# Performance work log

Measured on AMD Instinct MI355X. Metric: run time of the kernel, lower is better.

Reference implementation:

```python
import jax, jax.numpy as jnp
import numpy as np

CUBE_SIZE = 24
N_NEURONS = CUBE_SIZE ** 3  # 13824
INPUT_DIM = 512
OUTPUT_DIM = 1000
MAX_STEPS = 30
BATCH = 256


def _build_neighbor_indices(size: int) -> np.ndarray:
    """[N, 27] int32; invalid (out-of-cube) neighbors map to pad slot N."""
    n = size ** 3
    c = np.arange(size)
    z, y, x = np.meshgrid(c, c, c, indexing='ij')  # each [size,size,size]
    cols = []
    for dz in (-1, 0, 1):
        for dy in (-1, 0, 1):
            for dx in (-1, 0, 1):
                nz, ny, nx = z + dz, y + dy, x + dx
                valid = ((nz >= 0) & (nz < size) & (ny >= 0) & (ny < size)
                         & (nx >= 0) & (nx < size))
                idx = nz * size * size + ny * size + nx
                cols.append(np.where(valid, idx, n))
    return np.stack(cols, axis=-1).reshape(n, 27).astype(np.int32)


def setup_inputs() -> dict:
    key = jax.random.key(0)
    ks = jax.random.split(key, 4)
    # xavier-ish small init scales (gain 0.5 style)
    w_in = jax.random.normal(ks[0], (N_NEURONS, INPUT_DIM), jnp.float32) * 0.01
    w_local = jax.random.normal(ks[1], (N_NEURONS, 27), jnp.float32) * 0.1
    w_out = jax.random.normal(ks[2], (OUTPUT_DIM, N_NEURONS), jnp.float32) * 0.01
    x = jax.random.normal(ks[3], (BATCH, INPUT_DIM), jnp.float32)
    return {
        'x': x,
        'W_in_w': w_in,
        'W_in_b': jnp.zeros((N_NEURONS,), jnp.float32),
        'W_local': w_local,
        'W_out_w': w_out,
        'W_out_b': jnp.zeros((OUTPUT_DIM,), jnp.float32),
        'neighbor_indices': jnp.asarray(_build_neighbor_indices(CUBE_SIZE)),
    }


def reference(x, W_in_w, W_in_b, W_local, W_out_w, W_out_b, neighbor_indices):
    batch = x.shape[0]
    x_proj = x @ W_in_w.T + W_in_b  # [B, N]
    h0 = jnp.zeros((batch, N_NEURONS), x.dtype)
    pad = jnp.zeros((batch, 1), x.dtype)

    def step(h, _):
        h_padded = jnp.concatenate([h, pad], axis=1)        # [B, N+1]
        nbr = h_padded[:, neighbor_indices]                  # [B, N, 27]
        weighted = jnp.einsum('bnk,nk->bn', nbr, W_local)    # [B, N]
        return jnp.tanh(x_proj + weighted), None

    h, _ = jax.lax.scan(step, h0, None, length=MAX_STEPS)
    return h @ W_out_w.T + W_out_b  # [B, output_dim]
```

## Files before the change

kernel.cpp:

```cpp
#include <hip/hip_runtime.h>
#include <hip/hip_bf16.h>

#define NN   13824
#define BB   256
#define KDIM 512
#define ODIM 1000
#define CUBE 24
#define KS   16
#define ASTR 872

typedef short bf8 __attribute__((ext_vector_type(8)));
typedef float f32x4 __attribute__((ext_vector_type(4)));

__device__ __forceinline__ float fast_tanh(float a) {
    float e = __expf(2.0f * a);
    return 1.0f - 2.0f / (e + 1.0f);
}
__device__ __forceinline__ float bf_lo(unsigned u) { return __uint_as_float(u << 16); }
__device__ __forceinline__ float bf_hi(unsigned u) { return __uint_as_float(u & 0xffff0000u); }
__device__ __forceinline__ unsigned short bf_rne(float f) {
    unsigned u = __float_as_uint(f);
    u += 0x7fffu + ((u >> 16) & 1u);
    return (unsigned short)(u >> 16);
}
__device__ __forceinline__ unsigned pk_bf16(float lo, float hi) {
    union { __hip_bfloat162 h; unsigned u; } cv;
    cv.h = __float22bfloat162_rn(make_float2(lo, hi));
    return cv.u;
}
__device__ __forceinline__ bf8 cvt8(float4 a, float4 b) {
    union { bf8 v; unsigned u[4]; } r;
    r.u[0] = pk_bf16(a.x, a.y);
    r.u[1] = pk_bf16(a.z, a.w);
    r.u[2] = pk_bf16(b.x, b.y);
    r.u[3] = pk_bf16(b.z, b.w);
    return r.v;
}

__global__ __launch_bounds__(256) void xbf_kernel(
    const float* __restrict__ x, unsigned* __restrict__ xb)
{
    int i = blockIdx.x * 256 + threadIdx.x;
    float2 v = *(const float2*)&x[(size_t)i * 2];
    xb[i] = pk_bf16(v.x, v.y);
}

__global__ __launch_bounds__(256) void xproj_mfma(
    const float* __restrict__ w_in, const float* __restrict__ bias,
    const short* __restrict__ xbf, unsigned short* __restrict__ xp,
    unsigned short* __restrict__ h1)
{
    const int tid = threadIdx.x, w = tid >> 6, lane = tid & 63;
    const int quad = lane >> 4, l16 = lane & 15;
    const int n0 = blockIdx.x * 16;
    const float* __restrict__ arow = &w_in[(size_t)(n0 + l16) * KDIM];

    f32x4 acc[4] = {};

    int ka = quad * 8;
    float4 a0 = *(const float4*)&arow[ka];
    float4 a1 = *(const float4*)&arow[ka + 4];
    bf8 bb[4];
#pragma unroll
    for (int j = 0; j < 4; ++j)
        bb[j] = *(const bf8*)&xbf[(size_t)(w * 64 + j * 16 + l16) * KDIM + ka];

    for (int it = 0; it < 16; ++it) {
        float4 na0{}, na1{}; bf8 nb[4] = {};
        if (it < 15) {
            const int nka = ka + 32;
            na0 = *(const float4*)&arow[nka];
            na1 = *(const float4*)&arow[nka + 4];
#pragma unroll
            for (int j = 0; j < 4; ++j)
                nb[j] = *(const bf8*)&xbf[(size_t)(w * 64 + j * 16 + l16) * KDIM + nka];
        }
        bf8 af = cvt8(a0, a1);
#pragma unroll
        for (int j = 0; j < 4; ++j)
            acc[j] = __builtin_amdgcn_mfma_f32_16x16x32_bf16(af, bb[j], acc[j], 0, 0, 0);
        a0 = na0; a1 = na1;
#pragma unroll
        for (int j = 0; j < 4; ++j) bb[j] = nb[j];
        ka += 32;
    }

#pragma unroll
    for (int j = 0; j < 4; ++j) {
        const int b = w * 64 + j * 16 + l16;
#pragma unroll
        for (int r = 0; r < 4; ++r) {
            const int n = n0 + quad * 4 + r;
            const float v = acc[j][r] + bias[n];
            xp[(size_t)n * BB + b] = bf_rne(v);
            h1[(size_t)n * BB + b] = bf_rne(fast_tanh(v));
        }
    }
}

__device__ __forceinline__ void load_plane_f2(
    const unsigned* __restrict__ h32, int z, int y, int xx, int dof, float2* w9)
{
#pragma unroll
    for (int j = 0; j < 9; ++j) {
        const int dz = j / 3 - 1, dy = j % 3 - 1;
        const int zz = z + dz, yy = y + dy;
        const bool valid = (xx >= 0) & (xx < CUBE) & (zz >= 0) & (zz < CUBE) &
                           (yy >= 0) & (yy < CUBE);
        unsigned v = 0u;
        if (valid) v = h32[(size_t)((zz * 24 + yy) * 24 + xx) * 128 + dof];
        w9[j] = make_float2(bf_lo(v), bf_hi(v));
    }
}

__global__ __launch_bounds__(256) void step_kernel(
    const unsigned* __restrict__ hprev, const unsigned* __restrict__ xp,
    const float* __restrict__ wl, unsigned* __restrict__ hnext)
{
    const int tid  = threadIdx.x;
    const int wid  = __builtin_amdgcn_readfirstlane(tid >> 6);
    const int wvb  = wid & 1;
    const int yoff = wid >> 1;
    const int lane = tid & 63;

    const int bid   = blockIdx.x;
    const int zhi   = bid & 7;
    const int inner = bid >> 3;
    const int yp    = inner % 12;
    const int r     = inner / 12;
    const int xc    = r & 3;
    const int zlo   = r >> 2;
    const int z     = zhi * 3 + zlo;
    const int y     = yp * 2 + yoff;

    const int x0   = xc * 6;
    const int dof  = wvb * 64 + lane;

    float2 win[5][9];
    load_plane_f2(hprev, z, y, x0 - 1, dof, win[0]);
    load_plane_f2(hprev, z, y, x0,     dof, win[1]);
    load_plane_f2(hprev, z, y, x0 + 1, dof, win[2]);
    load_plane_f2(hprev, z, y, x0 + 2, dof, win[3]);

#pragma unroll
    for (int xi = 0; xi < 6; ++xi) {
        const int x = x0 + xi;
        if (xi <= 3)
            load_plane_f2(hprev, z, y, x + 3, dof, win[(xi + 4) % 5]);

        const int n = (z * 24 + y) * 24 + x;
        const float* __restrict__ wn = &wl[(size_t)n * 27];
        const unsigned xpv = xp[(size_t)n * 128 + dof];
        float2 acc = make_float2(bf_lo(xpv), bf_hi(xpv));

        const float2* pm = win[xi % 5];
        const float2* pc = win[(xi + 1) % 5];
        const float2* pp = win[(xi + 2) % 5];
#pragma unroll
        for (int j = 0; j < 9; ++j) {
            const float w0 = wn[3 * j + 0];
            const float w1 = wn[3 * j + 1];
            const float w2 = wn[3 * j + 2];
            acc.x += w0 * pm[j].x + w1 * pc[j].x + w2 * pp[j].x;
            acc.y += w0 * pm[j].y + w1 * pc[j].y + w2 * pp[j].y;
        }
        hnext[(size_t)n * 128 + dof] = pk_bf16(fast_tanh(acc.x), fast_tanh(acc.y));
    }
}

__global__ __launch_bounds__(256) void transpose_kernel(
    const unsigned* __restrict__ h32, unsigned* __restrict__ hT32)
{
    __shared__ unsigned short T[64][66];
    const int tid = threadIdx.x;
    const int rr = tid >> 2, g = tid & 3;
    const int k0 = blockIdx.x * 64, b0 = blockIdx.y * 64;
#pragma unroll
    for (int i = 0; i < 8; ++i) {
        unsigned d = h32[(size_t)(k0 + rr) * 128 + b0 / 2 + g * 8 + i];
        const int bl = (g * 8 + i) * 2;
        T[bl][rr]     = (unsigned short)(d & 0xffffu);
        T[bl + 1][rr] = (unsigned short)(d >> 16);
    }
    __syncthreads();
#pragma unroll
    for (int i = 0; i < 8; ++i) {
        const int kl = (g * 8 + i) * 2;
        unsigned d = (unsigned)T[rr][kl] | ((unsigned)T[rr][kl + 1] << 16);
        hT32[(size_t)(b0 + rr) * (NN / 2) + k0 / 2 + g * 8 + i] = d;
    }
}

__global__ __launch_bounds__(256) void outgemm_mfma(
    const float* __restrict__ wout, const short* __restrict__ hT,
    float* __restrict__ part)
{
    __shared__ unsigned short As[32 * ASTR];
    const int tid = threadIdx.x, w = tid >> 6, lane = tid & 63;
    const int quad = lane >> 4, l16 = lane & 15;
    const int kb = blockIdx.x * (NN / KS);
    const int o0 = blockIdx.y * 32;
    const int b0 = w * 64;

#pragma unroll
    for (int rr = 0; rr < 8; ++rr) {
        const int row = w * 8 + rr;
        const int o = o0 + row;
        const float* __restrict__ src = &wout[(size_t)o * NN + kb];
#pragma unroll
        for (int c = 0; c < 4; ++c) {
            const int col = c * 256 + lane * 4;
            if (c < 3 || lane < 24) {
                float4 v = {0.f, 0.f, 0.f, 0.f};
                if (o < ODIM) v = *(const float4*)&src[col];
                uint2 pk2 = make_uint2(pk_bf16(v.x, v.y), pk_bf16(v.z, v.w));
                *(uint2*)&As[(unsigned)row * ASTR + (unsigned)col] = pk2;
            }
        }
    }
    __syncthreads();

    f32x4 acc[2][4] = {};

    bf8 bb[4];
    {
        const int ka = kb + quad * 8;
#pragma unroll
        for (int j = 0; j < 4; ++j)
            bb[j] = *(const bf8*)&hT[(size_t)(b0 + j * 16 + l16) * NN + ka];
    }

    const int r0 = l16, r1 = 16 + l16;

    for (int kc = 0; kc < 27; ++kc) {
        bf8 nb[4] = {};
        if (kc < 26) {
            const int ka = kb + (kc + 1) * 32 + quad * 8;
#pragma unroll
            for (int j = 0; j < 4; ++j)
                nb[j] = *(const bf8*)&hT[(size_t)(b0 + j * 16 + l16) * NN + ka];
        }
        const int cs = kc * 32 + quad * 8;
        bf8 a0 = *(const bf8*)&As[(unsigned)r0 * ASTR + (unsigned)cs];
        bf8 a1 = *(const bf8*)&As[(unsigned)r1 * ASTR + (unsigned)cs];
#pragma unroll
        for (int j = 0; j < 4; ++j) {
            acc[0][j] = __builtin_amdgcn_mfma_f32_16x16x32_bf16(a0, bb[j], acc[0][j], 0, 0, 0);
            acc[1][j] = __builtin_amdgcn_mfma_f32_16x16x32_bf16(a1, bb[j], acc[1][j], 0, 0, 0);
        }
#pragma unroll
        for (int j = 0; j < 4; ++j) bb[j] = nb[j];
    }

#pragma unroll
    for (int i = 0; i < 2; ++i)
#pragma unroll
        for (int j = 0; j < 4; ++j) {
            const int b = b0 + j * 16 + l16;
#pragma unroll
            for (int r = 0; r < 4; ++r) {
                const int o = o0 + i * 16 + quad * 4 + r;
                part[((size_t)blockIdx.x * 1024 + o) * BB + b] = acc[i][j][r];
            }
        }
}

__global__ __launch_bounds__(256) void reduce_kernel(
    const float* __restrict__ part, const float* __restrict__ bias,
    float* __restrict__ out)
{
    const int o = blockIdx.x, b = threadIdx.x;
    float s = bias[o];
#pragma unroll
    for (int kc = 0; kc < KS; ++kc)
        s += part[((size_t)kc * 1024 + o) * BB + b];
    out[(size_t)b * ODIM + o] = s;
}

extern "C" void kernel_launch(void* const* d_in, const int* in_sizes, int n_in,
                              void* d_out, int out_size, void* d_ws, size_t ws_size,
                              hipStream_t stream)
{
    const float* x       = (const float*)d_in[0];
    const float* w_in    = (const float*)d_in[1];
    const float* b_in    = (const float*)d_in[2];
    const float* w_local = (const float*)d_in[3];
    const float* w_out   = (const float*)d_in[4];
    const float* b_out   = (const float*)d_in[5];
    float* out = (float*)d_out;

    char* p = (char*)d_ws;
    unsigned short* xp_bf = (unsigned short*)p;          p += (size_t)NN * BB * 2;
    unsigned short* hA    = (unsigned short*)p;          p += (size_t)NN * BB * 2;
    unsigned short* hB    = (unsigned short*)p;          p += (size_t)NN * BB * 2;
    unsigned short* hT    = (unsigned short*)p;          p += (size_t)NN * BB * 2;
    unsigned short* x_bf  = (unsigned short*)p;          p += (size_t)BB * KDIM * 2;
    float*          part  = (float*)p;

    xbf_kernel<<<256, 256, 0, stream>>>(x, (unsigned*)x_bf);
    xproj_mfma<<<864, 256, 0, stream>>>(w_in, b_in, (const short*)x_bf, xp_bf, hA);

    const unsigned* hp = (const unsigned*)hA;
    unsigned* hn = (unsigned*)hB;
    for (int s = 0; s < 29; ++s) {
        step_kernel<<<1152, 256, 0, stream>>>(hp, (const unsigned*)xp_bf, w_local, hn);
        unsigned* t = (unsigned*)hp; hp = hn; hn = t;
    }

    transpose_kernel<<<dim3(216, 4), 256, 0, stream>>>(hp, (unsigned*)hT);
    outgemm_mfma<<<dim3(KS, 32), 256, 0, stream>>>(w_out, (const short*)hT, part);
    reduce_kernel<<<ODIM, 256, 0, stream>>>(part, b_out, out);
}
```

Baseline: 552.9 us.

## Stage 3D halo tiles of hidden state in LDS for stencil step

The step kernel now loads a 6x6x6 halo tile (4x4x4 interior) of the previous hidden state for 64 batch pairs into shared memory, then each wave computes one z-slice of the tile from LDS. This replaces the old per-thread global sliding-window loads, cutting redundant global reads of neighbours. The grid drops from 1152 to 432 blocks, which may reduce occupancy and parallelism, and the 54 KB LDS tile limits blocks per CU. Separately, the xproj kernel converts its W_in row block to bf16 once into LDS instead of converting in registers inside the loop.

Result: slower. 986.3 us (+78.4%).

```diff
diff --git a/kernel.cpp b/kernel.cpp
--- a/kernel.cpp
+++ b/kernel.cpp
@@ -8,6 +8,7 @@
 #define CUBE 24
 #define KS   16
 #define ASTR 872
+#define XSTR 520
 
 typedef short bf8 __attribute__((ext_vector_type(8)));
 typedef float f32x4 __attribute__((ext_vector_type(4)));
@@ -28,14 +29,6 @@
     cv.h = __float22bfloat162_rn(make_float2(lo, hi));
     return cv.u;
 }
-__device__ __forceinline__ bf8 cvt8(float4 a, float4 b) {
-    union { bf8 v; unsigned u[4]; } r;
-    r.u[0] = pk_bf16(a.x, a.y);
-    r.u[1] = pk_bf16(a.z, a.w);
-    r.u[2] = pk_bf16(b.x, b.y);
-    r.u[3] = pk_bf16(b.z, b.w);
-    return r.v;
-}
 
 __global__ __launch_bounds__(256) void xbf_kernel(
     const float* __restrict__ x, unsigned* __restrict__ xb)
@@ -50,36 +43,45 @@
     const short* __restrict__ xbf, unsigned short* __restrict__ xp,
     unsigned short* __restrict__ h1)
 {
+    __shared__ unsigned short As[16 * XSTR];
     const int tid = threadIdx.x, w = tid >> 6, lane = tid & 63;
     const int quad = lane >> 4, l16 = lane & 15;
     const int n0 = blockIdx.x * 16;
-    const float* __restrict__ arow = &w_in[(size_t)(n0 + l16) * KDIM];
+
+#pragma unroll
+    for (int rr = 0; rr < 4; ++rr) {
+        const int row = w * 4 + rr;
+        const float* __restrict__ src = &w_in[(size_t)(n0 + row) * KDIM];
+#pragma unroll
+        for (int c = 0; c < 2; ++c) {
+            const int col = c * 256 + lane * 4;
+            float4 v = *(const float4*)&src[col];
+            uint2 pk2 = make_uint2(pk_bf16(v.x, v.y), pk_bf16(v.z, v.w));
+            *(uint2*)&As[row * XSTR + col] = pk2;
+        }
+    }
+    __syncthreads();
 
     f32x4 acc[4] = {};
 
     int ka = quad * 8;
-    float4 a0 = *(const float4*)&arow[ka];
-    float4 a1 = *(const float4*)&arow[ka + 4];
     bf8 bb[4];
 #pragma unroll
     for (int j = 0; j < 4; ++j)
         bb[j] = *(const bf8*)&xbf[(size_t)(w * 64 + j * 16 + l16) * KDIM + ka];
 
     for (int it = 0; it < 16; ++it) {
-        float4 na0{}, na1{}; bf8 nb[4] = {};
+        bf8 nb[4] = {};
         if (it < 15) {
             const int nka = ka + 32;
-            na0 = *(const float4*)&arow[nka];
-            na1 = *(const float4*)&arow[nka + 4];
 #pragma unroll
             for (int j = 0; j < 4; ++j)
                 nb[j] = *(const bf8*)&xbf[(size_t)(w * 64 + j * 16 + l16) * KDIM + nka];
         }
-        bf8 af = cvt8(a0, a1);
+        bf8 af = *(const bf8*)&As[l16 * XSTR + it * 32 + quad * 8];
 #pragma unroll
         for (int j = 0; j < 4; ++j)
             acc[j] = __builtin_amdgcn_mfma_f32_16x16x32_bf16(af, bb[j], acc[j], 0, 0, 0);
-        a0 = na0; a1 = na1;
 #pragma unroll
         for (int j = 0; j < 4; ++j) bb[j] = nb[j];
         ka += 32;
@@ -98,17 +100,14 @@
     }
 }
 
-__device__ __forceinline__ void load_plane_f2(
-    const unsigned* __restrict__ h32, int z, int y, int xx, int dof, float2* w9)
+__device__ __forceinline__ void ldplane_lds(
+    const unsigned* __restrict__ Ls, int zo, int yo, int p, int lane,
+    float2* w9)
 {
 #pragma unroll
     for (int j = 0; j < 9; ++j) {
-        const int dz = j / 3 - 1, dy = j % 3 - 1;
-        const int zz = z + dz, yy = y + dy;
-        const bool valid = (xx >= 0) & (xx < CUBE) & (zz >= 0) & (zz < CUBE) &
-                           (yy >= 0) & (yy < CUBE);
-        unsigned v = 0u;
-        if (valid) v = h32[(size_t)((zz * 24 + yy) * 24 + xx) * 128 + dof];
+        const int dz = j / 3, dy = j % 3;
+        const unsigned v = Ls[(((zo + dz) * 6 + (yo + dy)) * 6 + p) * 64 + lane];
         w9[j] = make_float2(bf_lo(v), bf_hi(v));
     }
 }
@@ -117,54 +116,66 @@
     const unsigned* __restrict__ hprev, const unsigned* __restrict__ xp,
     const float* __restrict__ wl, unsigned* __restrict__ hnext)
 {
+    __shared__ unsigned Ls[216 * 64];
     const int tid  = threadIdx.x;
-    const int wid  = __builtin_amdgcn_readfirstlane(tid >> 6);
-    const int wvb  = wid & 1;
-    const int yoff = wid >> 1;
+    const int w    = __builtin_amdgcn_readfirstlane(tid >> 6);
     const int lane = tid & 63;
 
-    const int bid   = blockIdx.x;
-    const int zhi   = bid & 7;
-    const int inner = bid >> 3;
-    const int yp    = inner % 12;
-    const int r     = inner / 12;
-    const int xc    = r & 3;
-    const int zlo   = r >> 2;
-    const int z     = zhi * 3 + zlo;
-    const int y     = yp * 2 + yoff;
-
-    const int x0   = xc * 6;
-    const int dof  = wvb * 64 + lane;
-
+    const int bid  = blockIdx.x;
+    const int half = bid & 1;
+    const int t    = bid >> 1;
+    const int tx   = t % 6;
+    const int ty   = (t / 6) % 6;
+    const int tz   = t / 36;
+    const int z0 = tz * 4, y0 = ty * 4, x0 = tx * 4;
+    const int dof = half * 64 + lane;
+
+#pragma unroll 6
+    for (int i = 0; i < 54; ++i) {
+        const int r  = w * 54 + i;
+        const int lx = r % 6, ly = (r / 6) % 6, lz = r / 36;
+        const int z = z0 - 1 + lz, y = y0 - 1 + ly, x = x0 - 1 + lx;
+        const bool valid = (z >= 0) & (z < CUBE) & (y >= 0) & (y < CUBE) &
+                           (x >= 0) & (x < CUBE);
+        unsigned v = 0u;
+        if (valid) v = hprev[(size_t)((z * 24 + y) * 24 + x) * 128 + dof];
+        Ls[r * 64 + lane] = v;
+    }
+    __syncthreads();
+
+    const int zo = w;
     float2 win[5][9];
-    load_plane_f2(hprev, z, y, x0 - 1, dof, win[0]);
-    load_plane_f2(hprev, z, y, x0,     dof, win[1]);
-    load_plane_f2(hprev, z, y, x0 + 1, dof, win[2]);
-    load_plane_f2(hprev, z, y, x0 + 2, dof, win[3]);
-
-#pragma unroll
-    for (int xi = 0; xi < 6; ++xi) {
-        const int x = x0 + xi;
-        if (xi <= 3)
-            load_plane_f2(hprev, z, y, x + 3, dof, win[(xi + 4) % 5]);
-
-        const int n = (z * 24 + y) * 24 + x;
-        const float* __restrict__ wn = &wl[(size_t)n * 27];
-        const unsigned xpv = xp[(size_t)n * 128 + dof];
-        float2 acc = make_float2(bf_lo(xpv), bf_hi(xpv));
-
-        const float2* pm = win[xi % 5];
-        const float2* pc = win[(xi + 1) % 5];
-        const float2* pp = win[(xi + 2) % 5];
-#pragma unroll
-        for (int j = 0; j < 9; ++j) {
-            const float w0 = wn[3 * j + 0];
-            const float w1 = wn[3 * j + 1];
-            const float w2 = wn[3 * j + 2];
-            acc.x += w0 * pm[j].x + w1 * pc[j].x + w2 * pp[j].x;
-            acc.y += w0 * pm[j].y + w1 * pc[j].y + w2 * pp[j].y;
-        }
-        hnext[(size_t)n * 128 + dof] = pk_bf16(fast_tanh(acc.x), fast_tanh(acc.y));
+#pragma unroll 1
+    for (int yo = 0; yo < 4; ++yo) {
+        ldplane_lds(Ls, zo, yo, 0, lane, win[0]);
+        ldplane_lds(Ls, zo, yo, 1, lane, win[1]);
+        ldplane_lds(Ls, zo, yo, 2, lane, win[2]);
+        ldplane_lds(Ls, zo, yo, 3, lane, win[3]);
+
+#pragma unroll
+        for (int xo = 0; xo < 4; ++xo) {
+            if (xo <= 1)
+                ldplane_lds(Ls, zo, yo, xo + 4, lane, win[(xo + 4) % 5]);
+
+            const int n = ((z0 + zo) * 24 + (y0 + yo)) * 24 + (x0 + xo);
+            const float* __restrict__ wn = &wl[(size_t)n * 27];
+            const unsigned xpv = xp[(size_t)n * 128 + dof];
+            float2 acc = make_float2(bf_lo(xpv), bf_hi(xpv));
+
+            const float2* pm = win[xo % 5];
+            const float2* pc = win[(xo + 1) % 5];
+            const float2* pp = win[(xo + 2) % 5];
+#pragma unroll
+            for (int j = 0; j < 9; ++j) {
+                const float w0 = wn[3 * j + 0];
+                const float w1 = wn[3 * j + 1];
+                const float w2 = wn[3 * j + 2];
+                acc.x += w0 * pm[j].x + w1 * pc[j].x + w2 * pp[j].x;
+                acc.y += w0 * pm[j].y + w1 * pc[j].y + w2 * pp[j].y;
+            }
+            hnext[(size_t)n * 128 + dof] =
+                pk_bf16(fast_tanh(acc.x), fast_tanh(acc.y));
+        }
     }
 }
 
@@ -303,7 +314,7 @@
     const unsigned* hp = (const unsigned*)hA;
     unsigned* hn = (unsigned*)hB;
     for (int s = 0; s < 29; ++s) {
-        step_kernel<<<1152, 256, 0, stream>>>(hp, (const unsigned*)xp_bf, w_local, hn);
+        step_kernel<<<432, 256, 0, stream>>>(hp, (const unsigned*)xp_bf, w_local, hn);
         unsigned* t = (unsigned*)hp; hp = hn; hn = t;
     }
 
```

## Stage W_in through LDS in xproj and retile output GEMM to 128-row blocks

Applied to the files above, without the earlier changes.

In xproj, each block now loads its 16 W_in rows coalesced, converts them to bf16 once into shared memory, and feeds the MFMAs from LDS instead of strided per-lane global loads. The output GEMM is restructured to 512-thread blocks covering 128 output rows, with the weight tile staged in two K phases so it fits in LDS. Each hT fragment now feeds 8 MFMA row tiles, cutting redundant hT reads. The cost is fewer blocks (128 instead of 512), an extra barrier between phases, and more accumulator registers per thread.

After: 553.8 us. Within noise of the previous version (+0.1%).

```diff
diff --git a/kernel.cpp b/kernel.cpp
--- a/kernel.cpp
+++ b/kernel.cpp
@@ -7,7 +7,8 @@
 #define ODIM 1000
 #define CUBE 24
 #define KS   16
-#define ASTR 872
+#define XSTR 520
+#define OSTR 456
 
 typedef short bf8 __attribute__((ext_vector_type(8)));
 typedef float f32x4 __attribute__((ext_vector_type(4)));
@@ -28,14 +29,6 @@
     cv.h = __float22bfloat162_rn(make_float2(lo, hi));
     return cv.u;
 }
-__device__ __forceinline__ bf8 cvt8(float4 a, float4 b) {
-    union { bf8 v; unsigned u[4]; } r;
-    r.u[0] = pk_bf16(a.x, a.y);
-    r.u[1] = pk_bf16(a.z, a.w);
-    r.u[2] = pk_bf16(b.x, b.y);
-    r.u[3] = pk_bf16(b.z, b.w);
-    return r.v;
-}
 
 __global__ __launch_bounds__(256) void xbf_kernel(
     const float* __restrict__ x, unsigned* __restrict__ xb)
@@ -50,36 +43,45 @@
     const short* __restrict__ xbf, unsigned short* __restrict__ xp,
     unsigned short* __restrict__ h1)
 {
+    __shared__ unsigned short As[16 * XSTR];
     const int tid = threadIdx.x, w = tid >> 6, lane = tid & 63;
     const int quad = lane >> 4, l16 = lane & 15;
     const int n0 = blockIdx.x * 16;
-    const float* __restrict__ arow = &w_in[(size_t)(n0 + l16) * KDIM];
+
+#pragma unroll
+    for (int rr = 0; rr < 4; ++rr) {
+        const int row = w * 4 + rr;
+        const float* __restrict__ src = &w_in[(size_t)(n0 + row) * KDIM];
+#pragma unroll
+        for (int c = 0; c < 2; ++c) {
+            const int col = c * 256 + lane * 4;
+            float4 v = *(const float4*)&src[col];
+            uint2 pk2 = make_uint2(pk_bf16(v.x, v.y), pk_bf16(v.z, v.w));
+            *(uint2*)&As[row * XSTR + col] = pk2;
+        }
+    }
+    __syncthreads();
 
     f32x4 acc[4] = {};
 
     int ka = quad * 8;
-    float4 a0 = *(const float4*)&arow[ka];
-    float4 a1 = *(const float4*)&arow[ka + 4];
     bf8 bb[4];
 #pragma unroll
     for (int j = 0; j < 4; ++j)
         bb[j] = *(const bf8*)&xbf[(size_t)(w * 64 + j * 16 + l16) * KDIM + ka];
 
     for (int it = 0; it < 16; ++it) {
-        float4 na0{}, na1{}; bf8 nb[4] = {};
+        bf8 nb[4] = {};
         if (it < 15) {
             const int nka = ka + 32;
-            na0 = *(const float4*)&arow[nka];
-            na1 = *(const float4*)&arow[nka + 4];
 #pragma unroll
             for (int j = 0; j < 4; ++j)
                 nb[j] = *(const bf8*)&xbf[(size_t)(w * 64 + j * 16 + l16) * KDIM + nka];
         }
-        bf8 af = cvt8(a0, a1);
+        bf8 af = *(const bf8*)&As[l16 * XSTR + it * 32 + quad * 8];
 #pragma unroll
         for (int j = 0; j < 4; ++j)
             acc[j] = __builtin_amdgcn_mfma_f32_16x16x32_bf16(af, bb[j], acc[j], 0, 0, 0);
-        a0 = na0; a1 = na1;
 #pragma unroll
         for (int j = 0; j < 4; ++j) bb[j] = nb[j];
         ka += 32;
@@ -191,76 +193,83 @@
     }
 }
 
-__global__ __launch_bounds__(256) void outgemm_mfma(
+__global__ __launch_bounds__(512) void outgemm_mfma(
     const float* __restrict__ wout, const short* __restrict__ hT,
     float* __restrict__ part)
 {
-    __shared__ unsigned short As[32 * ASTR];
+    __shared__ unsigned short As[128 * OSTR];
     const int tid = threadIdx.x, w = tid >> 6, lane = tid & 63;
     const int quad = lane >> 4, l16 = lane & 15;
     const int kb = blockIdx.x * (NN / KS);
-    const int o0 = blockIdx.y * 32;
-    const int b0 = w * 64;
-
-#pragma unroll
-    for (int rr = 0; rr < 8; ++rr) {
-        const int row = w * 8 + rr;
-        const int o = o0 + row;
-        const float* __restrict__ src = &wout[(size_t)o * NN + kb];
-#pragma unroll
-        for (int c = 0; c < 4; ++c) {
-            const int col = c * 256 + lane * 4;
-            if (c < 3 || lane < 24) {
+    const int o0 = blockIdx.y * 128;
+    const int b0 = w * 32;
+
+    f32x4 acc[8][2] = {};
+
+#pragma unroll 1
+    for (int ph = 0; ph < 2; ++ph) {
+        const int poff  = ph ? 448 : 0;
+        const int pcols = ph ? 416 : 448;
+        const int pkc   = ph ? 13 : 14;
+        if (ph) __syncthreads();
+
+#pragma unroll 4
+        for (int rr = 0; rr < 16; ++rr) {
+            const int row = w * 16 + rr;
+            const int o = o0 + row;
+            const float* __restrict__ src = &wout[(size_t)o * NN + kb + poff];
+            {
+                const int col = lane * 4;
                 float4 v = {0.f, 0.f, 0.f, 0.f};
                 if (o < ODIM) v = *(const float4*)&src[col];
-                uint2 pk2 = make_uint2(pk_bf16(v.x, v.y), pk_bf16(v.z, v.w));
-                *(uint2*)&As[(unsigned)row * ASTR + (unsigned)col] = pk2;
-            }
-        }
-    }
-    __syncthreads();
-
-    f32x4 acc[2][4] = {};
-
-    bf8 bb[4];
-    {
-        const int ka = kb + quad * 8;
-#pragma unroll
-        for (int j = 0; j < 4; ++j)
-            bb[j] = *(const bf8*)&hT[(size_t)(b0 + j * 16 + l16) * NN + ka];
-    }
-
-    const int r0 = l16, r1 = 16 + l16;
-
-    for (int kc = 0; kc < 27; ++kc) {
-        bf8 nb[4] = {};
-        if (kc < 26) {
-            const int ka = kb + (kc + 1) * 32 + quad * 8;
-#pragma unroll
-            for (int j = 0; j < 4; ++j)
-                nb[j] = *(const bf8*)&hT[(size_t)(b0 + j * 16 + l16) * NN + ka];
-        }
-        const int cs = kc * 32 + quad * 8;
-        bf8 a0 = *(const bf8*)&As[(unsigned)r0 * ASTR + (unsigned)cs];
-        bf8 a1 = *(const bf8*)&As[(unsigned)r1 * ASTR + (unsigned)cs];
-#pragma unroll
-        for (int j = 0; j < 4; ++j) {
-            acc[0][j] = __builtin_amdgcn_mfma_f32_16x16x32_bf16(a0, bb[j], acc[0][j], 0, 0, 0);
-            acc[1][j] = __builtin_amdgcn_mfma_f32_16x16x32_bf16(a1, bb[j], acc[1][j], 0, 0, 0);
-        }
-#pragma unroll
-        for (int j = 0; j < 4; ++j) bb[j] = nb[j];
-    }
-
-#pragma unroll
-    for (int i = 0; i < 2; ++i)
-#pragma unroll
-        for (int j = 0; j < 4; ++j) {
+                *(uint2*)&As[row * OSTR + col] =
+                    make_uint2(pk_bf16(v.x, v.y), pk_bf16(v.z, v.w));
+            }
+            {
+                const int col = 256 + lane * 4;
+                if (col < pcols) {
+                    float4 v = {0.f, 0.f, 0.f, 0.f};
+                    if (o < ODIM) v = *(const float4*)&src[col];
+                    *(uint2*)&As[row * OSTR + col] =
+                        make_uint2(pk_bf16(v.x, v.y), pk_bf16(v.z, v.w));
+                }
+            }
+        }
+        __syncthreads();
+
+        bf8 b0f, b1f;
+        {
+            const int ka = kb + poff + quad * 8;
+            b0f = *(const bf8*)&hT[(size_t)(b0 + l16) * NN + ka];
+            b1f = *(const bf8*)&hT[(size_t)(b0 + 16 + l16) * NN + ka];
+        }
+        for (int kc = 0; kc < pkc; ++kc) {
+            bf8 n0 = {}, n1 = {};
+            if (kc + 1 < pkc) {
+                const int ka = kb + poff + (kc + 1) * 32 + quad * 8;
+                n0 = *(const bf8*)&hT[(size_t)(b0 + l16) * NN + ka];
+                n1 = *(const bf8*)&hT[(size_t)(b0 + 16 + l16) * NN + ka];
+            }
+            const int cs = kc * 32 + quad * 8;
+#pragma unroll
+            for (int t = 0; t < 8; ++t) {
+                bf8 af = *(const bf8*)&As[(t * 16 + l16) * OSTR + cs];
+                acc[t][0] = __builtin_amdgcn_mfma_f32_16x16x32_bf16(af, b0f, acc[t][0], 0, 0, 0);
+                acc[t][1] = __builtin_amdgcn_mfma_f32_16x16x32_bf16(af, b1f, acc[t][1], 0, 0, 0);
+            }
+            b0f = n0; b1f = n1;
+        }
+    }
+
+#pragma unroll
+    for (int t = 0; t < 8; ++t)
+#pragma unroll
+        for (int j = 0; j < 2; ++j) {
             const int b = b0 + j * 16 + l16;
 #pragma unroll
             for (int r = 0; r < 4; ++r) {
-                const int o = o0 + i * 16 + quad * 4 + r;
-                part[((size_t)blockIdx.x * 1024 + o) * BB + b] = acc[i][j][r];
+                const int o = o0 + t * 16 + quad * 4 + r;
+                part[((size_t)blockIdx.x * 1024 + o) * BB + b] = acc[t][j][r];
             }
         }
 }
@@ -308,6 +317,6 @@
     }
 
     transpose_kernel<<<dim3(216, 4), 256, 0, stream>>>(hp, (unsigned*)hT);
-    outgemm_mfma<<<dim3(KS, 32), 256, 0, stream>>>(w_out, (const short*)hT, part);
+    outgemm_mfma<<<dim3(KS, 8), 512, 0, stream>>>(w_out, (const short*)hT, part);
     reduce_kernel<<<ODIM, 256, 0, stream>>>(part, b_out, out);
 }
```
